# Performance work log

Hardware: AMD Instinct MI355X
Metric: run time of the kernel (lower is better)

The kernel has to match this reference:

```python
import jax, jax.numpy as jnp
import numpy as np

N, E, G = 100000, 1600000, 64   # nodes, edges, graphs
IN, H, OUT = 32, 128, 3


def setup_inputs() -> dict:
    key = jax.random.key(0)
    ks = jax.random.split(key, 24)
    def w(k, i, o):
        return (jax.random.normal(k, (i, o), jnp.float32) / np.sqrt(i)).astype(jnp.float32)
    inp = {
        "x": jax.random.normal(ks[0], (N, IN), jnp.float32),
        "edge_index": jax.random.randint(ks[1], (2, E), 0, N, dtype=jnp.int32).astype(jnp.int64),
        "batch": jnp.sort(jax.random.randint(ks[2], (N,), 0, G, dtype=jnp.int32)).astype(jnp.int64),
        # SAGEConv layer 0 (in->hidden): lin_l (neighbors, with bias), lin_r (root, no bias)
        "Wl0": w(ks[3], IN, H), "bl0": jnp.zeros((H,), jnp.float32), "Wr0": w(ks[4], IN, H),
        # SAGEConv layers 1,2 (hidden->hidden)
        "Wl1": w(ks[5], H, H), "bl1": jnp.zeros((H,), jnp.float32), "Wr1": w(ks[6], H, H),
        "Wl2": w(ks[7], H, H), "bl2": jnp.zeros((H,), jnp.float32), "Wr2": w(ks[8], H, H),
        # output head
        "Wfc": w(ks[9], H, OUT), "bfc": jnp.zeros((OUT,), jnp.float32),
        # aux MLP on (dim1, dim3)
        "Wa1": w(ks[10], 2, H), "ba1": jnp.zeros((H,), jnp.float32),
        "Wa2": w(ks[11], H, H), "ba2": jnp.zeros((H,), jnp.float32),
        "Wao": w(ks[12], H, 1), "bao": jnp.zeros((1,), jnp.float32),
    }
    return inp


def _sage_conv(x, src, dst, Wl, bl, Wr):
    # PyG SAGEConv (mean aggr): out = lin_l(mean_{j in N(i)} x_j) + lin_r(x_i)
    msg = x[src]                                   # [E, d] gather
    agg = jax.ops.segment_sum(msg, dst, num_segments=N)
    cnt = jax.ops.segment_sum(jnp.ones((src.shape[0],), x.dtype), dst, num_segments=N)
    mean = agg / jnp.maximum(cnt, 1.0)[:, None]
    return mean @ Wl + bl + x @ Wr


def reference(x, edge_index, batch,
              Wl0, bl0, Wr0, Wl1, bl1, Wr1, Wl2, bl2, Wr2,
              Wfc, bfc, Wa1, ba1, Wa2, ba2, Wao, bao):
    src, dst = edge_index[0], edge_index[1]
    h = jax.nn.relu(_sage_conv(x, src, dst, Wl0, bl0, Wr0))   # dropout is identity in eval
    h = jax.nn.relu(_sage_conv(h, src, dst, Wl1, bl1, Wr1))
    h = jax.nn.relu(_sage_conv(h, src, dst, Wl2, bl2, Wr2))
    main = h @ Wfc + bfc                                      # [N, 3]
    dim1, dim3 = main[:, 0], main[:, 2]
    aux_in = jnp.stack([dim1, dim3], axis=-1)                 # [N, 2]
    a = jax.nn.relu(aux_in @ Wa1 + ba1)
    a = jax.nn.relu(a @ Wa2 + ba2)
    aux_out = (a @ Wao + bao)[:, 0]                           # [N]
    final = jnp.stack([dim1, aux_out, dim3], axis=-1)         # [N, 3]
    # global mean pool over graph ids
    s = jax.ops.segment_sum(final, batch, num_segments=G)
    c = jax.ops.segment_sum(jnp.ones((final.shape[0],), final.dtype), batch, num_segments=G)
    return s / jnp.maximum(c, 1.0)[:, None]                   # [G, 3]
```

## Files before the change

kernel.cpp:

```cpp
#include <hip/hip_runtime.h>

#define NR 128
#define PART_CH 4096
typedef unsigned short ushortT;
typedef __attribute__((ext_vector_type(8))) short short8;
typedef __attribute__((ext_vector_type(4))) float float4v;
typedef __attribute__((ext_vector_type(2))) float float2v;

__device__ __forceinline__ unsigned short f32_to_bf16_rne(float f) {
    unsigned u = __float_as_uint(f);
    unsigned r = (u + 0x7fffu + ((u >> 16) & 1u)) >> 16;
    return (unsigned short)r;
}

__device__ __forceinline__ unsigned char f32_to_fp8(float f) {
    return (unsigned char)(__builtin_amdgcn_cvt_pk_fp8_f32(f, f, 0, false) & 0xff);
}

__device__ __forceinline__ void accum8(float* acc, uint4 v) {
    unsigned u[4] = {v.x, v.y, v.z, v.w};
#pragma unroll
    for (int q = 0; q < 4; q++) {
        acc[2 * q]     += __uint_as_float(u[q] << 16);
        acc[2 * q + 1] += __uint_as_float(u[q] & 0xffff0000u);
    }
}

__device__ __forceinline__ void accum32_fp8(float* ag, uint4 A, uint4 B) {
    unsigned w[8] = {A.x, A.y, A.z, A.w, B.x, B.y, B.z, B.w};
#pragma unroll
    for (int m = 0; m < 8; m++) {
        float2v lo = __builtin_amdgcn_cvt_pk_f32_fp8(w[m], false);
        float2v hi = __builtin_amdgcn_cvt_pk_f32_fp8(w[m], true);
        ag[4 * m + 0] += lo.x;
        ag[4 * m + 1] += lo.y;
        ag[4 * m + 2] += hi.x;
        ag[4 * m + 3] += hi.y;
    }
}


__launch_bounds__(256)
__global__ void bucket_count(const int* __restrict__ dst, int* __restrict__ bcnt, int E, int NB) {
    __shared__ int h[1024];
    int t = threadIdx.x;
    for (int j = t; j < NB; j += 256) h[j] = 0;
    __syncthreads();
    int e0 = blockIdx.x * PART_CH;
    int e1 = min(e0 + PART_CH, E);
    for (int base = e0; base < e1; base += 2048) {
        int idx = base + t;
        int d[8];
        int cnt = 0;
#pragma unroll
        for (int u = 0; u < 8; u++) {
            int e = idx + u * 256;
            if (e < e1) d[cnt++] = dst[e];
        }
        for (int u = 0; u < cnt; u++) atomicAdd(&h[d[u] >> 7], 1);
    }
    __syncthreads();
    for (int j = t; j < NB; j += 256) {
        int v = h[j];
        if (v) atomicAdd(&bcnt[j], v);
    }
}

__launch_bounds__(256)
__global__ void bucket_scan(const int* __restrict__ bcnt, int* __restrict__ bstart,
                            int* __restrict__ gcur, int NB, int E) {
    __shared__ int sh[256];
    int t = threadIdx.x;
    int v[4];
    int tot = 0;
#pragma unroll
    for (int j = 0; j < 4; j++) {
        int idx = t * 4 + j;
        v[j] = (idx < NB) ? bcnt[idx] : 0;
        tot += v[j];
    }
    sh[t] = tot;
    __syncthreads();
    for (int off = 1; off < 256; off <<= 1) {
        int add = (t >= off) ? sh[t - off] : 0;
        __syncthreads();
        sh[t] += add;
        __syncthreads();
    }
    int run = sh[t] - tot;
#pragma unroll
    for (int j = 0; j < 4; j++) {
        int idx = t * 4 + j;
        if (idx < NB) { bstart[idx] = run; gcur[idx] = run; }
        run += v[j];
    }
    if (t == 0) bstart[NB] = E;
}

__launch_bounds__(256)
__global__ void partition_edges(const int* __restrict__ src, const int* __restrict__ dst,
                                int* __restrict__ gcur, unsigned* __restrict__ packed,
                                int E, int NB) {
    __shared__ int hist[1024];
    __shared__ int base[1024];
    int t = threadIdx.x;
    int e0 = blockIdx.x * PART_CH;
    int e1 = min(e0 + PART_CH, E);
    for (int j = t; j < NB; j += 256) hist[j] = 0;
    __syncthreads();
    for (int bb = e0; bb < e1; bb += 2048) {
        int idx = bb + t;
        int d[8];
        int cnt = 0;
#pragma unroll
        for (int u = 0; u < 8; u++) {
            int e = idx + u * 256;
            if (e < e1) d[cnt++] = dst[e];
        }
        for (int u = 0; u < cnt; u++) atomicAdd(&hist[d[u] >> 7], 1);
    }
    __syncthreads();
    for (int j = t; j < NB; j += 256) {
        int h = hist[j];
        base[j] = h ? atomicAdd(&gcur[j], h) : 0;
    }
    __syncthreads();
    for (int j = t; j < NB; j += 256) hist[j] = base[j];
    __syncthreads();
    for (int bb = e0; bb < e1; bb += 2048) {
        int idx = bb + t;
        int d[8], s[8];
        int cnt = 0;
#pragma unroll
        for (int u = 0; u < 8; u++) {
            int e = idx + u * 256;
            if (e < e1) { d[cnt] = dst[e]; s[cnt] = src[e]; cnt++; }
        }
        for (int u = 0; u < cnt; u++) {
            int dd = d[u];
            int pos = atomicAdd(&hist[dd >> 7], 1);
            packed[pos] = (unsigned)s[u] | ((unsigned)(dd & (NR - 1)) << 17);
        }
    }
}

__launch_bounds__(256)
__global__ void bucket_sort(const unsigned* __restrict__ packed, const int* __restrict__ bstart,
                            int* __restrict__ row_start, int* __restrict__ srcs, int N) {
    __shared__ int cnt[NR];
    __shared__ int sc[NR];
    __shared__ int cur[NR];
    int b = blockIdx.x, t = threadIdx.x;
    int nb0 = b * NR;
    int nnode = min(NR, N - nb0);
    int lo = bstart[b], hi = bstart[b + 1];
    if (t < NR) cnt[t] = 0;
    __syncthreads();
    for (int bb = lo; bb < hi; bb += 2048) {
        int idx = bb + t;
        unsigned pk[8];
        int c = 0;
#pragma unroll
        for (int u = 0; u < 8; u++) {
            int e = idx + u * 256;
            if (e < hi) pk[c++] = packed[e];
        }
        for (int u = 0; u < c; u++) atomicAdd(&cnt[pk[u] >> 17], 1);
    }
    __syncthreads();
    if (t < NR) sc[t] = cnt[t];
    __syncthreads();
    for (int off = 1; off < NR; off <<= 1) {
        int add = (t >= off && t < NR) ? sc[t - off] : 0;
        __syncthreads();
        if (t < NR) sc[t] += add;
        __syncthreads();
    }
    if (t < nnode) {
        int s = lo + sc[t] - cnt[t];
        row_start[nb0 + t] = s;
        cur[t] = s;
    }
    if (t == 0 && nb0 + nnode == N) row_start[N] = hi;
    __syncthreads();
    for (int bb = lo; bb < hi; bb += 2048) {
        int idx = bb + t;
        unsigned pk[8];
        int c = 0;
#pragma unroll
        for (int u = 0; u < 8; u++) {
            int e = idx + u * 256;
            if (e < hi) pk[c++] = packed[e];
        }
        for (int u = 0; u < c; u++) {
            int pos = atomicAdd(&cur[pk[u] >> 17], 1);
            srcs[pos] = (int)(pk[u] & 0x1FFFFu);
        }
    }
}


__global__ void prep_fused(const float* __restrict__ x, ushortT* __restrict__ xbf, int n4,
                           const float* __restrict__ Wl0, const float* __restrict__ Wr0,
                           const float* __restrict__ Wl1, const float* __restrict__ Wr1,
                           const float* __restrict__ Wl2, const float* __restrict__ Wr2,
                           const float* __restrict__ Wa2,
                           ushortT* __restrict__ Wt0, ushortT* __restrict__ Wt1,
                           ushortT* __restrict__ Wt2, ushortT* __restrict__ Wa2t) {
    int tid0 = blockIdx.x * 256 + threadIdx.x;
    if (tid0 < n4) {
        float4 v = ((const float4*)x)[tid0];
        ushort4 o;
        o.x = f32_to_bf16_rne(v.x);
        o.y = f32_to_bf16_rne(v.y);
        o.z = f32_to_bf16_rne(v.z);
        o.w = f32_to_bf16_rne(v.w);
        ((ushort4*)xbf)[tid0] = o;
        return;
    }
    int tid = tid0 - n4;
    if (tid < 8192) {
        int col = tid >> 6, k = tid & 63;
        float v = (k < 32) ? Wl0[k * 128 + col] : Wr0[(k - 32) * 128 + col];
        Wt0[col * 64 + ((k + 8 * col) & 63)] = f32_to_bf16_rne(v);
    } else if (tid < 8192 + 32768) {
        int j = tid - 8192;
        int col = j >> 8, k = j & 255;
        float v = (k < 128) ? Wl1[k * 128 + col] : Wr1[(k - 128) * 128 + col];
        Wt1[(k >> 7) * 16384 + col * 128 + (((k & 127) + 8 * col) & 127)] = f32_to_bf16_rne(v);
    } else if (tid < 8192 + 65536) {
        int j = tid - 8192 - 32768;
        int col = j >> 8, k = j & 255;
        float v = (k < 128) ? Wl2[k * 128 + col] : Wr2[(k - 128) * 128 + col];
        Wt2[(k >> 7) * 16384 + col * 128 + (((k & 127) + 8 * col) & 127)] = f32_to_bf16_rne(v);
    } else if (tid < 8192 + 65536 + 16384) {
        int j = tid - 8192 - 65536;
        int col = j >> 7, k = j & 127;
        Wa2t[col * 128 + ((k + 8 * col) & 127)] = f32_to_bf16_rne(Wa2[k * 128 + col]);
    }
}


__device__ __forceinline__ void gather_fp8(const uint4* __restrict__ hp,
                                           const int* __restrict__ srcs,
                                           int lo, int deg, int q, float* ag) {
    if (deg <= 0) return;
    int last = lo + deg - 1;
    int nb = (deg + 3) >> 2;
    uint4 A[8], B[8];
#pragma unroll
    for (int u = 0; u < 4; u++) {
        size_t bs = (size_t)srcs[min(lo + u, last)] * 8 + q * 2;
        A[2 * u] = hp[bs];
        A[2 * u + 1] = hp[bs + 1];
    }
    int b = 0;
    while (true) {
        if (b + 1 < nb) {
#pragma unroll
            for (int u = 0; u < 4; u++) {
                size_t bs = (size_t)srcs[min(lo + (b + 1) * 4 + u, last)] * 8 + q * 2;
                B[2 * u] = hp[bs];
                B[2 * u + 1] = hp[bs + 1];
            }
        }
        int rem = deg - b * 4;
#pragma unroll
        for (int u = 0; u < 4; u++)
            if (u < rem) accum32_fp8(ag, A[2 * u], A[2 * u + 1]);
        b++;
        if (b >= nb) break;
        if (b + 1 < nb) {
#pragma unroll
            for (int u = 0; u < 4; u++) {
                size_t bs = (size_t)srcs[min(lo + (b + 1) * 4 + u, last)] * 8 + q * 2;
                A[2 * u] = hp[bs];
                A[2 * u + 1] = hp[bs + 1];
            }
        }
        rem = deg - b * 4;
#pragma unroll
        for (int u = 0; u < 4; u++)
            if (u < rem) accum32_fp8(ag, B[2 * u], B[2 * u + 1]);
        b++;
        if (b >= nb) break;
    }
}

__device__ __forceinline__ void gather_bf16(const uint4* __restrict__ xp,
                                            const int* __restrict__ srcs,
                                            int lo, int deg, int q, float* ag) {
    if (deg <= 0) return;
    int last = lo + deg - 1;
    int nb = (deg + 7) >> 3;
    uint4 A[8], B[8];
#pragma unroll
    for (int u = 0; u < 8; u++) A[u] = xp[(size_t)srcs[min(lo + u, last)] * 4 + q];
    int b = 0;
    while (true) {
        if (b + 1 < nb) {
#pragma unroll
            for (int u = 0; u < 8; u++)
                B[u] = xp[(size_t)srcs[min(lo + (b + 1) * 8 + u, last)] * 4 + q];
        }
        int rem = deg - b * 8;
#pragma unroll
        for (int u = 0; u < 8; u++)
            if (u < rem) accum8(ag, A[u]);
        b++;
        if (b >= nb) break;
        if (b + 1 < nb) {
#pragma unroll
            for (int u = 0; u < 8; u++)
                A[u] = xp[(size_t)srcs[min(lo + (b + 1) * 8 + u, last)] * 4 + q];
        }
        rem = deg - b * 8;
#pragma unroll
        for (int u = 0; u < 8; u++)
            if (u < rem) accum8(ag, B[u]);
        b++;
        if (b >= nb) break;
    }
}


template <int KH, bool IN_FP8>
__device__ __forceinline__ void gemm_agg_body(
        const void* __restrict__ gat, const ushortT* __restrict__ Ah,
        const int* __restrict__ srcs, const int* __restrict__ rs,
        const ushortT* __restrict__ Wt, const float* __restrict__ bias,
        ushortT* __restrict__ outbf, unsigned char* __restrict__ outf8, int n) {
    constexpr int NKS = KH / 32;
    constexpr int KTH = (KH == 32) ? 64 : 128;
    __shared__ __attribute__((aligned(16))) ushortT sW[128 * KTH];
    int t = threadIdx.x;
    {
        const uint4* Wg = (const uint4*)Wt;
        uint4* Ws = (uint4*)sW;
#pragma unroll
        for (int j = 0; j < (128 * KTH / 8) / 256; j++) Ws[t + j * 256] = Wg[t + j * 256];
    }
    int wv = t >> 6, lane = t & 63;
    int q = lane >> 4, cid = lane & 15;
    int row = blockIdx.x * 64 + wv * 16 + cid;
    int rc = min(row, n - 1);

    float ag[NKS * 8];
#pragma unroll
    for (int j = 0; j < NKS * 8; j++) ag[j] = 0.f;
    int lo = rs[rc], deg = rs[rc + 1] - lo;
    if constexpr (IN_FP8) gather_fp8((const uint4*)gat, srcs, lo, deg, q, ag);
    else                  gather_bf16((const uint4*)gat, srcs, lo, deg, q, ag);
    float inv = 1.0f / (float)max(deg, 1);
    short8 am[NKS];
#pragma unroll
    for (int ks = 0; ks < NKS; ks++)
#pragma unroll
        for (int j = 0; j < 8; j++) am[ks][j] = (short)f32_to_bf16_rne(ag[ks * 8 + j] * inv);
    __syncthreads();

    float4v acc[8];
#pragma unroll
    for (int j = 0; j < 8; j++) acc[j] = (float4v){0.f, 0.f, 0.f, 0.f};
    int pbase = q * 8 + 8 * cid;
#pragma unroll
    for (int ks = 0; ks < NKS; ks++) {
        int p = (ks * 32 + pbase) & (KTH - 1);
#pragma unroll
        for (int j = 0; j < 8; ++j) {
            short8 b = *(const short8*)(sW + (j * 16 + cid) * KTH + p);
            acc[j] = __builtin_amdgcn_mfma_f32_16x16x32_bf16(am[ks], b, acc[j], 0, 0, 0);
        }
    }
    if constexpr (KH == 32) {
        short8 ah = *(const short8*)(Ah + (size_t)rc * 32 + q * 8);
        int p = (32 + pbase) & 63;
#pragma unroll
        for (int j = 0; j < 8; ++j) {
            short8 b = *(const short8*)(sW + (j * 16 + cid) * 64 + p);
            acc[j] = __builtin_amdgcn_mfma_f32_16x16x32_bf16(ah, b, acc[j], 0, 0, 0);
        }
    } else {
        short8 ah[4];
#pragma unroll
        for (int ks = 0; ks < 4; ks++)
            ah[ks] = *(const short8*)(Ah + (size_t)rc * 128 + ks * 32 + q * 8);
        __syncthreads();
        {
            const uint4* Wg = (const uint4*)(Wt + 128 * 128);
            uint4* Ws = (uint4*)sW;
#pragma unroll
            for (int j = 0; j < 8; j++) Ws[t + j * 256] = Wg[t + j * 256];
        }
        __syncthreads();
#pragma unroll
        for (int ks = 0; ks < 4; ks++) {
            int p = (ks * 32 + pbase) & 127;
#pragma unroll
            for (int j = 0; j < 8; ++j) {
                short8 b = *(const short8*)(sW + (j * 16 + cid) * 128 + p);
                acc[j] = __builtin_amdgcn_mfma_f32_16x16x32_bf16(ah[ks], b, acc[j], 0, 0, 0);
            }
        }
    }
    float bo[8];
#pragma unroll
    for (int j = 0; j < 8; ++j) bo[j] = bias[j * 16 + cid];
    int orow = blockIdx.x * 64 + wv * 16 + q * 4;
#pragma unroll
    for (int rr = 0; rr < 4; ++rr) {
        int r = orow + rr;
        if (r < n) {
#pragma unroll
            for (int j = 0; j < 8; ++j) {
                int col = j * 16 + cid;
                float v = fmaxf(acc[j][rr] + bo[j], 0.f);
                outbf[(size_t)r * 128 + col] = f32_to_bf16_rne(v);
                int pc = ((col >> 3) & 3) * 32 + ((col >> 5) << 3) + (col & 7);
                outf8[(size_t)r * 128 + pc] = f32_to_fp8(v);
            }
        }
    }
}

__launch_bounds__(256, 2)
__global__ void gemm_agg32(const void* __restrict__ gat, const ushortT* __restrict__ Ah,
                           const int* __restrict__ srcs, const int* __restrict__ rs,
                           const ushortT* __restrict__ Wt, const float* __restrict__ bias,
                           ushortT* __restrict__ outbf, unsigned char* __restrict__ outf8, int n) {
    gemm_agg_body<32, false>(gat, Ah, srcs, rs, Wt, bias, outbf, outf8, n);
}

__launch_bounds__(256, 2)
__global__ void gemm_agg128(const void* __restrict__ gat, const ushortT* __restrict__ Ah,
                            const int* __restrict__ srcs, const int* __restrict__ rs,
                            const ushortT* __restrict__ Wt, const float* __restrict__ bias,
                            ushortT* __restrict__ outbf, unsigned char* __restrict__ outf8, int n) {
    gemm_agg_body<128, true>(gat, Ah, srcs, rs, Wt, bias, outbf, outf8, n);
}


__launch_bounds__(256, 2)
__global__ void gemm_agg_fin(const void* __restrict__ gat, const ushortT* __restrict__ Ah,
                             const int* __restrict__ srcs, const int* __restrict__ rs,
                             const ushortT* __restrict__ Wt, const float* __restrict__ bias,
                             const float* __restrict__ Wfc, const float* __restrict__ bfc,
                             const ushortT* __restrict__ Wa2t, const float* __restrict__ Wa1,
                             const float* __restrict__ ba1, const float* __restrict__ ba2,
                             const float* __restrict__ Wao, const float* __restrict__ bao,
                             float* __restrict__ fin, int n) {
    __shared__ __attribute__((aligned(16))) ushortT sW[128 * 128];
    __shared__ float sD1[64], sD3[64];
    __shared__ float sWa1a[128], sWa1b[128], sBa1[128];
    int t = threadIdx.x;
    {
        const uint4* Wg = (const uint4*)Wt;
        uint4* Ws = (uint4*)sW;
#pragma unroll
        for (int j = 0; j < 8; j++) Ws[t + j * 256] = Wg[t + j * 256];
    }
    if (t < 128) { sWa1a[t] = Wa1[t]; sWa1b[t] = Wa1[128 + t]; sBa1[t] = ba1[t]; }
    int wv = t >> 6, lane = t & 63;
    int q = lane >> 4, cid = lane & 15;
    int row = blockIdx.x * 64 + wv * 16 + cid;
    int rc = min(row, n - 1);

    float ag[32];
#pragma unroll
    for (int j = 0; j < 32; j++) ag[j] = 0.f;
    int lo = rs[rc], deg = rs[rc + 1] - lo;
    gather_fp8((const uint4*)gat, srcs, lo, deg, q, ag);
    float inv = 1.0f / (float)max(deg, 1);
    short8 am[4];
#pragma unroll
    for (int ks = 0; ks < 4; ks++)
#pragma unroll
        for (int j = 0; j < 8; j++) am[ks][j] = (short)f32_to_bf16_rne(ag[ks * 8 + j] * inv);
    __syncthreads();

    float4v acc[8];
#pragma unroll
    for (int j = 0; j < 8; j++) acc[j] = (float4v){0.f, 0.f, 0.f, 0.f};
    int pbase = q * 8 + 8 * cid;
#pragma unroll
    for (int ks = 0; ks < 4; ks++) {
        int p = (ks * 32 + pbase) & 127;
#pragma unroll
        for (int j = 0; j < 8; ++j) {
            short8 b = *(const short8*)(sW + (j * 16 + cid) * 128 + p);
            acc[j] = __builtin_amdgcn_mfma_f32_16x16x32_bf16(am[ks], b, acc[j], 0, 0, 0);
        }
    }
    short8 ah[4];
#pragma unroll
    for (int ks = 0; ks < 4; ks++)
        ah[ks] = *(const short8*)(Ah + (size_t)rc * 128 + ks * 32 + q * 8);
    __syncthreads();
    {
        const uint4* Wg = (const uint4*)(Wt + 128 * 128);
        uint4* Ws = (uint4*)sW;
#pragma unroll
        for (int j = 0; j < 8; j++) Ws[t + j * 256] = Wg[t + j * 256];
    }
    __syncthreads();
#pragma unroll
    for (int ks = 0; ks < 4; ks++) {
        int p = (ks * 32 + pbase) & 127;
#pragma unroll
        for (int j = 0; j < 8; ++j) {
            short8 b = *(const short8*)(sW + (j * 16 + cid) * 128 + p);
            acc[j] = __builtin_amdgcn_mfma_f32_16x16x32_bf16(ah[ks], b, acc[j], 0, 0, 0);
        }
    }

    float bo[8], w1[8], w3[8];
#pragma unroll
    for (int j = 0; j < 8; ++j) {
        int col = j * 16 + cid;
        bo[j] = bias[col];
        w1[j] = Wfc[col * 3 + 0];
        w3[j] = Wfc[col * 3 + 2];
    }
    float bfc0 = bfc[0], bfc2 = bfc[2];
#pragma unroll
    for (int rr = 0; rr < 4; ++rr) {
        float p1 = 0.f, p3 = 0.f;
#pragma unroll
        for (int j = 0; j < 8; ++j) {
            float v = fmaxf(acc[j][rr] + bo[j], 0.f);
            p1 += v * w1[j];
            p3 += v * w3[j];
        }
        p1 += __shfl_xor(p1, 1, 64); p3 += __shfl_xor(p3, 1, 64);
        p1 += __shfl_xor(p1, 2, 64); p3 += __shfl_xor(p3, 2, 64);
        p1 += __shfl_xor(p1, 4, 64); p3 += __shfl_xor(p3, 4, 64);
        p1 += __shfl_xor(p1, 8, 64); p3 += __shfl_xor(p3, 8, 64);
        if (cid == 0) {
            int rowl = wv * 16 + q * 4 + rr;
            float d1 = p1 + bfc0, d3 = p3 + bfc2;
            sD1[rowl] = d1;
            sD3[rowl] = d3;
            int r = blockIdx.x * 64 + rowl;
            if (r < n) {
                fin[(size_t)r * 3 + 0] = d1;
                fin[(size_t)r * 3 + 2] = d3;
            }
        }
    }
    __syncthreads();
    {
        const uint4* Wg = (const uint4*)Wa2t;
        uint4* Ws = (uint4*)sW;
#pragma unroll
        for (int j = 0; j < 8; j++) Ws[t + j * 256] = Wg[t + j * 256];
    }
    __syncthreads();

    int rl = wv * 16 + cid;
    float d1a = sD1[rl], d3a = sD3[rl];
    float4v hacc[8];
#pragma unroll
    for (int j = 0; j < 8; j++) hacc[j] = (float4v){0.f, 0.f, 0.f, 0.f};
#pragma unroll
    for (int ks = 0; ks < 4; ++ks) {
        int k0 = ks * 32 + q * 8;
        short8 a0;
#pragma unroll
        for (int j = 0; j < 8; ++j) {
            int k = k0 + j;
            float v0 = fmaxf(fmaf(d1a, sWa1a[k], fmaf(d3a, sWa1b[k], sBa1[k])), 0.f);
            a0[j] = (short)f32_to_bf16_rne(v0);
        }
        int p = (ks * 32 + pbase) & 127;
#pragma unroll
        for (int j = 0; j < 8; ++j) {
            short8 b = *(const short8*)(sW + (j * 16 + cid) * 128 + p);
            hacc[j] = __builtin_amdgcn_mfma_f32_16x16x32_bf16(a0, b, hacc[j], 0, 0, 0);
        }
    }
    float b2[8], wo[8];
#pragma unroll
    for (int j = 0; j < 8; ++j) {
        int col = j * 16 + cid;
        b2[j] = ba2[col];
        wo[j] = Wao[col];
    }
    float bao0 = bao[0];
#pragma unroll
    for (int rr = 0; rr < 4; ++rr) {
        float s = 0.f;
#pragma unroll
        for (int j = 0; j < 8; ++j) s += fmaxf(hacc[j][rr] + b2[j], 0.f) * wo[j];
        s += __shfl_xor(s, 1, 64);
        s += __shfl_xor(s, 2, 64);
        s += __shfl_xor(s, 4, 64);
        s += __shfl_xor(s, 8, 64);
        int r = blockIdx.x * 64 + wv * 16 + q * 4 + rr;
        if (cid == 0 && r < n) fin[(size_t)r * 3 + 1] = s + bao0;
    }
}


__global__ void pool_kernel(const float* __restrict__ fin, const int* __restrict__ batch,
                            float* __restrict__ out, int n) {
    int g = blockIdx.x, t = threadIdx.x;
    int lo = 0, hi = n;
    while (lo < hi) { int mid = (lo + hi) >> 1; if (batch[mid] < g) lo = mid + 1; else hi = mid; }
    int start = lo;
    lo = 0; hi = n;
    while (lo < hi) { int mid = (lo + hi) >> 1; if (batch[mid] < g + 1) lo = mid + 1; else hi = mid; }
    int end = lo;
    float s0 = 0.f, s1 = 0.f, s2 = 0.f;
    for (int i = start + t; i < end; i += 256) {
        s0 += fin[(size_t)i * 3 + 0];
        s1 += fin[(size_t)i * 3 + 1];
        s2 += fin[(size_t)i * 3 + 2];
    }
    __shared__ float r0[256], r1[256], r2[256];
    r0[t] = s0; r1[t] = s1; r2[t] = s2;
    __syncthreads();
    for (int off = 128; off > 0; off >>= 1) {
        if (t < off) { r0[t] += r0[t + off]; r1[t] += r1[t + off]; r2[t] += r2[t + off]; }
        __syncthreads();
    }
    if (t == 0) {
        float c = (float)max(end - start, 1);
        out[g * 3 + 0] = r0[0] / c;
        out[g * 3 + 1] = r1[0] / c;
        out[g * 3 + 2] = r2[0] / c;
    }
}


extern "C" void kernel_launch(void* const* d_in, const int* in_sizes, int n_in,
                              void* d_out, int out_size, void* d_ws, size_t ws_size,
                              hipStream_t stream) {
    const float* x    = (const float*)d_in[0];
    const int*   ei   = (const int*)d_in[1];
    const int*   batch= (const int*)d_in[2];
    const float* Wl0  = (const float*)d_in[3];
    const float* bl0  = (const float*)d_in[4];
    const float* Wr0  = (const float*)d_in[5];
    const float* Wl1  = (const float*)d_in[6];
    const float* bl1  = (const float*)d_in[7];
    const float* Wr1  = (const float*)d_in[8];
    const float* Wl2  = (const float*)d_in[9];
    const float* bl2  = (const float*)d_in[10];
    const float* Wr2  = (const float*)d_in[11];
    const float* Wfc  = (const float*)d_in[12];
    const float* bfc  = (const float*)d_in[13];
    const float* Wa1  = (const float*)d_in[14];
    const float* ba1  = (const float*)d_in[15];
    const float* Wa2  = (const float*)d_in[16];
    const float* ba2  = (const float*)d_in[17];
    const float* Wao  = (const float*)d_in[18];
    const float* bao  = (const float*)d_in[19];

    const int N = in_sizes[0] / 32;
    const int E = in_sizes[1] / 2;
    const int G = out_size / 3;
    const int* src = ei;
    const int* dst = ei + E;
    float* out = (float*)d_out;
    const int NB = (N + NR - 1) / NR;

    char* p = (char*)d_ws;
    auto carve = [&](size_t bytes) {
        void* r = (void*)p;
        p += (bytes + 255) & ~(size_t)255;
        return r;
    };
    int*           bcnt     = (int*)carve((size_t)NB * 4);
    int*           bstart   = (int*)carve((size_t)(NB + 1) * 4);
    int*           gcur     = (int*)carve((size_t)NB * 4);
    int*           row_start= (int*)carve((size_t)(N + 1) * 4);
    unsigned*      packed   = (unsigned*)carve((size_t)E * 4);
    int*           srcs     = (int*)carve((size_t)E * 4);
    ushortT*       xbf      = (ushortT*)carve((size_t)N * 32 * 2);
    ushortT*       hbf0     = (ushortT*)carve((size_t)N * 128 * 2);
    ushortT*       hbf1     = (ushortT*)carve((size_t)N * 128 * 2);
    unsigned char* hf8_0    = (unsigned char*)carve((size_t)N * 128);
    unsigned char* hf8_1    = (unsigned char*)carve((size_t)N * 128);
    float*         fin      = (float*)carve((size_t)N * 3 * 4);
    ushortT*       Wt0      = (ushortT*)carve((size_t)128 * 64 * 2);
    ushortT*       Wt1      = (ushortT*)carve((size_t)128 * 256 * 2);
    ushortT*       Wt2      = (ushortT*)carve((size_t)128 * 256 * 2);
    ushortT*       Wa2t     = (ushortT*)carve((size_t)128 * 128 * 2);

    const int gemm_grid = (N + 63) / 64;
    const int part_grid = (E + PART_CH - 1) / PART_CH;
    const int n4 = N * 32 / 4;

    prep_fused<<<(n4 + 90112 + 255) / 256, 256, 0, stream>>>(
        x, xbf, n4, Wl0, Wr0, Wl1, Wr1, Wl2, Wr2, Wa2, Wt0, Wt1, Wt2, Wa2t);

    hipMemsetAsync(bcnt, 0, (size_t)NB * 4, stream);
    bucket_count<<<part_grid, 256, 0, stream>>>(dst, bcnt, E, NB);
    bucket_scan<<<1, 256, 0, stream>>>(bcnt, bstart, gcur, NB, E);
    partition_edges<<<part_grid, 256, 0, stream>>>(src, dst, gcur, packed, E, NB);
    bucket_sort<<<NB, 256, 0, stream>>>(packed, bstart, row_start, srcs, N);

    gemm_agg32<<<gemm_grid, 256, 0, stream>>>(
        (const void*)xbf, xbf, srcs, row_start, Wt0, bl0, hbf0, hf8_0, N);
    gemm_agg128<<<gemm_grid, 256, 0, stream>>>(
        (const void*)hf8_0, hbf0, srcs, row_start, Wt1, bl1, hbf1, hf8_1, N);
    gemm_agg_fin<<<gemm_grid, 256, 0, stream>>>(
        (const void*)hf8_1, hbf1, srcs, row_start, Wt2, bl2, Wfc, bfc,
        Wa2t, Wa1, ba1, ba2, Wao, bao, fin, N);

    pool_kernel<<<G, 256, 0, stream>>>(fin, batch, out, N);
}
```

Baseline: 331.3 us.

## Halve LDS weight tiles to 64-K slices and shrink gather prefetch depth

Weight matrices are re-laid out into 64-wide K slices so each block holds only a 16 KB shared-memory tile, staged in four (or two) passes with syncs. The aim is to cut LDS and register use so more blocks fit per CU. The gather loops now prefetch fewer neighbors per batch and preload source indices one batch ahead, which lowers register pressure. The cost is more __syncthreads and weight reloads per block, plus less memory-level parallelism per thread in the gathers.

```diff
diff --git a/kernel.cpp b/kernel.cpp
--- a/kernel.cpp
+++ b/kernel.cpp
@@ -227,16 +227,16 @@
         int j = tid - 8192;
         int col = j >> 8, k = j & 255;
         float v = (k < 128) ? Wl1[k * 128 + col] : Wr1[(k - 128) * 128 + col];
-        Wt1[(k >> 7) * 16384 + col * 128 + (((k & 127) + 8 * col) & 127)] = f32_to_bf16_rne(v);
+        Wt1[(k >> 6) * 8192 + col * 64 + (((k & 63) + 8 * col) & 63)] = f32_to_bf16_rne(v);
     } else if (tid < 8192 + 65536) {
         int j = tid - 8192 - 32768;
         int col = j >> 8, k = j & 255;
         float v = (k < 128) ? Wl2[k * 128 + col] : Wr2[(k - 128) * 128 + col];
-        Wt2[(k >> 7) * 16384 + col * 128 + (((k & 127) + 8 * col) & 127)] = f32_to_bf16_rne(v);
+        Wt2[(k >> 6) * 8192 + col * 64 + (((k & 63) + 8 * col) & 63)] = f32_to_bf16_rne(v);
     } else if (tid < 8192 + 65536 + 16384) {
         int j = tid - 8192 - 65536;
         int col = j >> 7, k = j & 127;
-        Wa2t[col * 128 + ((k + 8 * col) & 127)] = f32_to_bf16_rne(Wa2[k * 128 + col]);
+        Wa2t[(k >> 6) * 8192 + col * 64 + (((k & 63) + 8 * col) & 63)] = f32_to_bf16_rne(Wa2[k * 128 + col]);
     }
 }
 
@@ -246,44 +246,49 @@
                                            int lo, int deg, int q, float* ag) {
     if (deg <= 0) return;
     int last = lo + deg - 1;
-    int nb = (deg + 3) >> 2;
-    uint4 A[8], B[8];
-#pragma unroll
-    for (int u = 0; u < 4; u++) {
-        size_t bs = (size_t)srcs[min(lo + u, last)] * 8 + q * 2;
-        A[2 * u] = hp[bs];
-        A[2 * u + 1] = hp[bs + 1];
-    }
-    int b = 0;
-    while (true) {
-        if (b + 1 < nb) {
-#pragma unroll
-            for (int u = 0; u < 4; u++) {
-                size_t bs = (size_t)srcs[min(lo + (b + 1) * 4 + u, last)] * 8 + q * 2;
-                B[2 * u] = hp[bs];
-                B[2 * u + 1] = hp[bs + 1];
-            }
-        }
-        int rem = deg - b * 4;
-#pragma unroll
-        for (int u = 0; u < 4; u++)
-            if (u < rem) accum32_fp8(ag, A[2 * u], A[2 * u + 1]);
-        b++;
-        if (b >= nb) break;
-        if (b + 1 < nb) {
-#pragma unroll
-            for (int u = 0; u < 4; u++) {
-                size_t bs = (size_t)srcs[min(lo + (b + 1) * 4 + u, last)] * 8 + q * 2;
-                A[2 * u] = hp[bs];
-                A[2 * u + 1] = hp[bs + 1];
-            }
-        }
-        rem = deg - b * 4;
-#pragma unroll
-        for (int u = 0; u < 4; u++)
-            if (u < rem) accum32_fp8(ag, B[2 * u], B[2 * u + 1]);
-        b++;
-        if (b >= nb) break;
+    int nb = (deg + 1) >> 1;
+    int sA0, sA1, sB0, sB1;
+    uint4 A[4], B[4];
+    sA0 = srcs[lo];
+    sA1 = srcs[min(lo + 1, last)];
+    sB0 = srcs[min(lo + 2, last)];
+    sB1 = srcs[min(lo + 3, last)];
+    {
+        size_t b0 = (size_t)sA0 * 8 + q * 2;
+        size_t b1 = (size_t)sA1 * 8 + q * 2;
+        A[0] = hp[b0]; A[1] = hp[b0 + 1];
+        A[2] = hp[b1]; A[3] = hp[b1 + 1];
+    }
+    for (int b = 0; b < nb; b++) {
+        if (!(b & 1)) {
+            if (b + 1 < nb) {
+                size_t b0 = (size_t)sB0 * 8 + q * 2;
+                size_t b1 = (size_t)sB1 * 8 + q * 2;
+                B[0] = hp[b0]; B[1] = hp[b0 + 1];
+                B[2] = hp[b1]; B[3] = hp[b1 + 1];
+            }
+            if (b + 2 < nb) {
+                sA0 = srcs[min(lo + (b + 2) * 2, last)];
+                sA1 = srcs[min(lo + (b + 2) * 2 + 1, last)];
+            }
+            int rem = deg - b * 2;
+            accum32_fp8(ag, A[0], A[1]);
+            if (rem > 1) accum32_fp8(ag, A[2], A[3]);
+        } else {
+            if (b + 1 < nb) {
+                size_t b0 = (size_t)sA0 * 8 + q * 2;
+                size_t b1 = (size_t)sA1 * 8 + q * 2;
+                A[0] = hp[b0]; A[1] = hp[b0 + 1];
+                A[2] = hp[b1]; A[3] = hp[b1 + 1];
+            }
+            if (b + 2 < nb) {
+                sB0 = srcs[min(lo + (b + 2) * 2, last)];
+                sB1 = srcs[min(lo + (b + 2) * 2 + 1, last)];
+            }
+            int rem = deg - b * 2;
+            accum32_fp8(ag, B[0], B[1]);
+            if (rem > 1) accum32_fp8(ag, B[2], B[3]);
+        }
     }
 }
 
@@ -292,37 +297,53 @@
                                             int lo, int deg, int q, float* ag) {
     if (deg <= 0) return;
     int last = lo + deg - 1;
-    int nb = (deg + 7) >> 3;
-    uint4 A[8], B[8];
-#pragma unroll
-    for (int u = 0; u < 8; u++) A[u] = xp[(size_t)srcs[min(lo + u, last)] * 4 + q];
-    int b = 0;
-    while (true) {
-        if (b + 1 < nb) {
-#pragma unroll
-            for (int u = 0; u < 8; u++)
-                B[u] = xp[(size_t)srcs[min(lo + (b + 1) * 8 + u, last)] * 4 + q];
-        }
-        int rem = deg - b * 8;
-#pragma unroll
-        for (int u = 0; u < 8; u++)
-            if (u < rem) accum8(ag, A[u]);
-        b++;
-        if (b >= nb) break;
-        if (b + 1 < nb) {
-#pragma unroll
-            for (int u = 0; u < 8; u++)
-                A[u] = xp[(size_t)srcs[min(lo + (b + 1) * 8 + u, last)] * 4 + q];
-        }
-        rem = deg - b * 8;
-#pragma unroll
-        for (int u = 0; u < 8; u++)
-            if (u < rem) accum8(ag, B[u]);
-        b++;
-        if (b >= nb) break;
-    }
-}
-
+    int nb = (deg + 3) >> 2;
+    int sA[4], sB[4];
+    uint4 A[4], B[4];
+#pragma unroll
+    for (int u = 0; u < 4; u++) sA[u] = srcs[min(lo + u, last)];
+#pragma unroll
+    for (int u = 0; u < 4; u++) sB[u] = srcs[min(lo + 4 + u, last)];
+#pragma unroll
+    for (int u = 0; u < 4; u++) A[u] = xp[(size_t)sA[u] * 4 + q];
+    for (int b = 0; b < nb; b++) {
+        if (!(b & 1)) {
+            if (b + 1 < nb) {
+#pragma unroll
+                for (int u = 0; u < 4; u++) B[u] = xp[(size_t)sB[u] * 4 + q];
+            }
+            if (b + 2 < nb) {
+#pragma unroll
+                for (int u = 0; u < 4; u++) sA[u] = srcs[min(lo + (b + 2) * 4 + u, last)];
+            }
+            int rem = deg - b * 4;
+#pragma unroll
+            for (int u = 0; u < 4; u++)
+                if (u < rem) accum8(ag, A[u]);
+        } else {
+            if (b + 1 < nb) {
+#pragma unroll
+                for (int u = 0; u < 4; u++) A[u] = xp[(size_t)sA[u] * 4 + q];
+            }
+            if (b + 2 < nb) {
+#pragma unroll
+                for (int u = 0; u < 4; u++) sB[u] = srcs[min(lo + (b + 2) * 4 + u, last)];
+            }
+            int rem = deg - b * 4;
+#pragma unroll
+            for (int u = 0; u < 4; u++)
+                if (u < rem) accum8(ag, B[u]);
+        }
+    }
+}
+
+
+__device__ __forceinline__ void stage_copy(ushortT* sW, const ushortT* Wq, int t) {
+    const uint4* Wg = (const uint4*)Wq;
+    uint4* Ws = (uint4*)sW;
+#pragma unroll
+    for (int j = 0; j < 4; j++) Ws[t + j * 256] = Wg[t + j * 256];
+}
 
 template <int KH, bool IN_FP8>
 __device__ __forceinline__ void gemm_agg_body(
@@ -331,15 +352,9 @@
         const ushortT* __restrict__ Wt, const float* __restrict__ bias,
         ushortT* __restrict__ outbf, unsigned char* __restrict__ outf8, int n) {
     constexpr int NKS = KH / 32;
-    constexpr int KTH = (KH == 32) ? 64 : 128;
-    __shared__ __attribute__((aligned(16))) ushortT sW[128 * KTH];
+    __shared__ __attribute__((aligned(16))) ushortT sW[128 * 64];
     int t = threadIdx.x;
-    {
-        const uint4* Wg = (const uint4*)Wt;
-        uint4* Ws = (uint4*)sW;
-#pragma unroll
-        for (int j = 0; j < (128 * KTH / 8) / 256; j++) Ws[t + j * 256] = Wg[t + j * 256];
-    }
+    stage_copy(sW, Wt, t);
     int wv = t >> 6, lane = t & 63;
     int q = lane >> 4, cid = lane & 15;
     int row = blockIdx.x * 64 + wv * 16 + cid;
@@ -357,49 +372,50 @@
     for (int ks = 0; ks < NKS; ks++)
 #pragma unroll
         for (int j = 0; j < 8; j++) am[ks][j] = (short)f32_to_bf16_rne(ag[ks * 8 + j] * inv);
+    short8 ah[NKS];
+#pragma unroll
+    for (int ks = 0; ks < NKS; ks++)
+        ah[ks] = *(const short8*)(Ah + (size_t)rc * KH + ks * 32 + q * 8);
     __syncthreads();
 
     float4v acc[8];
 #pragma unroll
     for (int j = 0; j < 8; j++) acc[j] = (float4v){0.f, 0.f, 0.f, 0.f};
     int pbase = q * 8 + 8 * cid;
-#pragma unroll
-    for (int ks = 0; ks < NKS; ks++) {
-        int p = (ks * 32 + pbase) & (KTH - 1);
-#pragma unroll
-        for (int j = 0; j < 8; ++j) {
-            short8 b = *(const short8*)(sW + (j * 16 + cid) * KTH + p);
-            acc[j] = __builtin_amdgcn_mfma_f32_16x16x32_bf16(am[ks], b, acc[j], 0, 0, 0);
-        }
-    }
     if constexpr (KH == 32) {
-        short8 ah = *(const short8*)(Ah + (size_t)rc * 32 + q * 8);
-        int p = (32 + pbase) & 63;
-#pragma unroll
-        for (int j = 0; j < 8; ++j) {
-            short8 b = *(const short8*)(sW + (j * 16 + cid) * 64 + p);
-            acc[j] = __builtin_amdgcn_mfma_f32_16x16x32_bf16(ah, b, acc[j], 0, 0, 0);
+        {
+            int p = pbase & 63;
+#pragma unroll
+            for (int j = 0; j < 8; ++j) {
+                short8 b = *(const short8*)(sW + (j * 16 + cid) * 64 + p);
+                acc[j] = __builtin_amdgcn_mfma_f32_16x16x32_bf16(am[0], b, acc[j], 0, 0, 0);
+            }
+        }
+        {
+            int p = (32 + pbase) & 63;
+#pragma unroll
+            for (int j = 0; j < 8; ++j) {
+                short8 b = *(const short8*)(sW + (j * 16 + cid) * 64 + p);
+                acc[j] = __builtin_amdgcn_mfma_f32_16x16x32_bf16(ah[0], b, acc[j], 0, 0, 0);
+            }
         }
     } else {
-        short8 ah[4];
-#pragma unroll
-        for (int ks = 0; ks < 4; ks++)
-            ah[ks] = *(const short8*)(Ah + (size_t)rc * 128 + ks * 32 + q * 8);
-        __syncthreads();
-        {
-            const uint4* Wg = (const uint4*)(Wt + 128 * 128);
-            uint4* Ws = (uint4*)sW;
-#pragma unroll
-            for (int j = 0; j < 8; j++) Ws[t + j * 256] = Wg[t + j * 256];
-        }
-        __syncthreads();
-#pragma unroll
-        for (int ks = 0; ks < 4; ks++) {
-            int p = (ks * 32 + pbase) & 127;
-#pragma unroll
-            for (int j = 0; j < 8; ++j) {
-                short8 b = *(const short8*)(sW + (j * 16 + cid) * 128 + p);
-                acc[j] = __builtin_amdgcn_mfma_f32_16x16x32_bf16(ah[ks], b, acc[j], 0, 0, 0);
+#pragma unroll
+        for (int st = 0; st < 4; st++) {
+            if (st > 0) {
+                __syncthreads();
+                stage_copy(sW, Wt + st * 8192, t);
+                __syncthreads();
+            }
+#pragma unroll
+            for (int ksl = 0; ksl < 2; ksl++) {
+                short8 a = (st < 2) ? am[st * 2 + ksl] : ah[(st - 2) * 2 + ksl];
+                int p = (ksl * 32 + pbase) & 63;
+#pragma unroll
+                for (int j = 0; j < 8; ++j) {
+                    short8 b = *(const short8*)(sW + (j * 16 + cid) * 64 + p);
+                    acc[j] = __builtin_amdgcn_mfma_f32_16x16x32_bf16(a, b, acc[j], 0, 0, 0);
+                }
             }
         }
     }
@@ -449,16 +465,11 @@
                              const float* __restrict__ ba1, const float* __restrict__ ba2,
                              const float* __restrict__ Wao, const float* __restrict__ bao,
                              float* __restrict__ fin, int n) {
-    __shared__ __attribute__((aligned(16))) ushortT sW[128 * 128];
+    __shared__ __attribute__((aligned(16))) ushortT sW[128 * 64];
     __shared__ float sD1[64], sD3[64];
     __shared__ float sWa1a[128], sWa1b[128], sBa1[128];
     int t = threadIdx.x;
-    {
-        const uint4* Wg = (const uint4*)Wt;
-        uint4* Ws = (uint4*)sW;
-#pragma unroll
-        for (int j = 0; j < 8; j++) Ws[t + j * 256] = Wg[t + j * 256];
-    }
+    stage_copy(sW, Wt, t);
     if (t < 128) { sWa1a[t] = Wa1[t]; sWa1b[t] = Wa1[128 + t]; sBa1[t] = ba1[t]; }
     int wv = t >> 6, lane = t & 63;
     int q = lane >> 4, cid = lane & 15;
@@ -476,6 +487,10 @@
     for (int ks = 0; ks < 4; ks++)
 #pragma unroll
         for (int j = 0; j < 8; j++) am[ks][j] = (short)f32_to_bf16_rne(ag[ks * 8 + j] * inv);
+    short8 ah[4];
+#pragma unroll
+    for (int ks = 0; ks < 4; ks++)
+        ah[ks] = *(const short8*)(Ah + (size_t)rc * 128 + ks * 32 + q * 8);
     __syncthreads();
 
     float4v acc[8];
@@ -483,33 +498,21 @@
     for (int j = 0; j < 8; j++) acc[j] = (float4v){0.f, 0.f, 0.f, 0.f};
     int pbase = q * 8 + 8 * cid;
 #pragma unroll
-    for (int ks = 0; ks < 4; ks++) {
-        int p = (ks * 32 + pbase) & 127;
-#pragma unroll
-        for (int j = 0; j < 8; ++j) {
-            short8 b = *(const short8*)(sW + (j * 16 + cid) * 128 + p);
-            acc[j] = __builtin_amdgcn_mfma_f32_16x16x32_bf16(am[ks], b, acc[j], 0, 0, 0);
-        }
-    }
-    short8 ah[4];
-#pragma unroll
-    for (int ks = 0; ks < 4; ks++)
-        ah[ks] = *(const short8*)(Ah + (size_t)rc * 128 + ks * 32 + q * 8);
-    __syncthreads();
-    {
-        const uint4* Wg = (const uint4*)(Wt + 128 * 128);
-        uint4* Ws = (uint4*)sW;
-#pragma unroll
-        for (int j = 0; j < 8; j++) Ws[t + j * 256] = Wg[t + j * 256];
-    }
-    __syncthreads();
-#pragma unroll
-    for (int ks = 0; ks < 4; ks++) {
-        int p = (ks * 32 + pbase) & 127;
-#pragma unroll
-        for (int j = 0; j < 8; ++j) {
-            short8 b = *(const short8*)(sW + (j * 16 + cid) * 128 + p);
-            acc[j] = __builtin_amdgcn_mfma_f32_16x16x32_bf16(ah[ks], b, acc[j], 0, 0, 0);
+    for (int st = 0; st < 4; st++) {
+        if (st > 0) {
+            __syncthreads();
+            stage_copy(sW, Wt + st * 8192, t);
+            __syncthreads();
+        }
+#pragma unroll
+        for (int ksl = 0; ksl < 2; ksl++) {
+            short8 a = (st < 2) ? am[st * 2 + ksl] : ah[(st - 2) * 2 + ksl];
+            int p = (ksl * 32 + pbase) & 63;
+#pragma unroll
+            for (int j = 0; j < 8; ++j) {
+                short8 b = *(const short8*)(sW + (j * 16 + cid) * 64 + p);
+                acc[j] = __builtin_amdgcn_mfma_f32_16x16x32_bf16(a, b, acc[j], 0, 0, 0);
+            }
         }
     }
 
@@ -548,13 +551,6 @@
         }
     }
     __syncthreads();
-    {
-        const uint4* Wg = (const uint4*)Wa2t;
-        uint4* Ws = (uint4*)sW;
-#pragma unroll
-        for (int j = 0; j < 8; j++) Ws[t + j * 256] = Wg[t + j * 256];
-    }
-    __syncthreads();
 
     int rl = wv * 16 + cid;
     float d1a = sD1[rl], d3a = sD3[rl];
@@ -562,20 +558,26 @@
 #pragma unroll
     for (int j = 0; j < 8; j++) hacc[j] = (float4v){0.f, 0.f, 0.f, 0.f};
 #pragma unroll
-    for (int ks = 0; ks < 4; ++ks) {
-        int k0 = ks * 32 + q * 8;
-        short8 a0;
-#pragma unroll
-        for (int j = 0; j < 8; ++j) {
-            int k = k0 + j;
-            float v0 = fmaxf(fmaf(d1a, sWa1a[k], fmaf(d3a, sWa1b[k], sBa1[k])), 0.f);
-            a0[j] = (short)f32_to_bf16_rne(v0);
-        }
-        int p = (ks * 32 + pbase) & 127;
-#pragma unroll
-        for (int j = 0; j < 8; ++j) {
-            short8 b = *(const short8*)(sW + (j * 16 + cid) * 128 + p);
-            hacc[j] = __builtin_amdgcn_mfma_f32_16x16x32_bf16(a0, b, hacc[j], 0, 0, 0);
+    for (int hs = 0; hs < 2; hs++) {
+        if (hs > 0) __syncthreads();
+        stage_copy(sW, Wa2t + hs * 8192, t);
+        __syncthreads();
+#pragma unroll
+        for (int ksl = 0; ksl < 2; ++ksl) {
+            int k0 = hs * 64 + ksl * 32 + q * 8;
+            short8 a0;
+#pragma unroll
+            for (int j = 0; j < 8; ++j) {
+                int k = k0 + j;
+                float v0 = fmaxf(fmaf(d1a, sWa1a[k], fmaf(d3a, sWa1b[k], sBa1[k])), 0.f);
+                a0[j] = (short)f32_to_bf16_rne(v0);
+            }
+            int p = (ksl * 32 + pbase) & 63;
+#pragma unroll
+            for (int j = 0; j < 8; ++j) {
+                short8 b = *(const short8*)(sW + (j * 16 + cid) * 64 + p);
+                hacc[j] = __builtin_amdgcn_mfma_f32_16x16x32_bf16(a0, b, hacc[j], 0, 0, 0);
+            }
         }
     }
     float b2[8], wo[8];
```

Result: no change. 336.2 us (+1.5%).
